# Performance work log

Hardware: AMD Instinct MI355X
Metric: run time of the kernel (lower is better)

## Reference

```python
import jax, jax.numpy as jnp
import numpy as np

N_BLOCKS = 96
N = N_BLOCKS ** 2          # number of image blocks = n_blocks^2
D = 1024                   # feature dim (fixed by Linear(1024+1, 128))
EPS_COS = 1e-6             # eps of F.cosine_similarity
EPS_BN = 1e-5              # BatchNorm1d eps


def setup_inputs() -> dict:
    key = jax.random.key(0)
    ks = jax.random.split(key, 6)
    return {
        "features": jax.random.normal(ks[0], (N, D), dtype=jnp.float32),
        "scores": jax.random.uniform(ks[1], (N,), dtype=jnp.float32),
        "W1": jax.random.normal(ks[2], (D + 1, 128), dtype=jnp.float32) * 0.03,
        "b1": jnp.zeros((128,), jnp.float32),
        "g1": jnp.ones((128,), jnp.float32),
        "be1": jnp.zeros((128,), jnp.float32),
        "W2": jax.random.normal(ks[3], (128, 64), dtype=jnp.float32) * 0.08,
        "b2": jnp.zeros((64,), jnp.float32),
        "g2": jnp.ones((64,), jnp.float32),
        "be2": jnp.zeros((64,), jnp.float32),
        "W3": jax.random.normal(ks[4], (64, 1), dtype=jnp.float32) * 0.12,
        "b3": jnp.zeros((1,), jnp.float32),
    }


def _gaussian_similarity(features):
    # Vectorized form of the O(N^2) pairwise loop:
    #   cos_ij = <f_i, f_j> / max(|f_i||f_j|, eps)
    #   sigma^2 = D * (0.5 + 0.5 * cos)  ->  2*sigma^2 = D * (1 + cos)
    #   sim_ij = exp(-|f_i - f_j|^2 / (2*sigma^2)),  sim_ii = 1
    sq = jnp.sum(features * features, axis=-1)          # [N] squared norms
    gram = features @ features.T                          # [N, N] big GEMM
    norms = jnp.sqrt(sq)
    cos = gram / jnp.maximum(norms[:, None] * norms[None, :], EPS_COS)
    d2 = jnp.maximum(sq[:, None] + sq[None, :] - 2.0 * gram, 0.0)
    denom = jnp.maximum(jnp.float32(D) * (1.0 + cos), EPS_COS)
    sim = jnp.exp(-d2 / denom)
    eye = jnp.eye(sim.shape[0], dtype=bool)
    return jnp.where(eye, jnp.float32(1.0), sim)


def _bn_eval(h, gamma, beta):
    # BatchNorm1d in eval mode with init running stats (mean=0, var=1).
    return gamma * (h / jnp.sqrt(1.0 + EPS_BN)) + beta


def reference(features, scores, W1, b1, g1, be1, W2, b2, g2, be2, W3, b3):
    sim = _gaussian_similarity(features)                  # [N, N]
    x = jnp.concatenate([features, scores[:, None]], axis=1)  # [N, D+1]
    h = jax.nn.relu(_bn_eval(x @ W1 + b1, g1, be1))       # [N, 128]
    h = jax.nn.relu(_bn_eval(h @ W2 + b2, g2, be2))       # [N, 64]
    agg = jax.nn.sigmoid(h @ W3 + b3)[:, 0]               # [N]
    sim_mean = jnp.mean(sim, axis=1)                      # [N]
    # Torch broadcast [N,1] * [N] -> [N,N], then .mean() == mean(agg)*mean(sim_mean)
    return jnp.mean(agg) * jnp.mean(sim_mean)


if __name__ == "__main__":
    out = reference(**setup_inputs())
    print(out)
```

## Files before the change

kernel.cpp:

```cpp
#include <hip/hip_runtime.h>

#define N_IMG 9216
#define DFEAT 1024
#define NBR2 72
#define NPAIR4 2628

typedef __attribute__((ext_vector_type(8))) short short8;
typedef __attribute__((ext_vector_type(4))) float floatx4;
typedef __attribute__((ext_vector_type(16))) float floatx16;
typedef __attribute__((ext_vector_type(4))) int intx4;
typedef __attribute__((ext_vector_type(8))) int intx8;

#define C1F 0.0014088818759657845f
#define C2F 0.05308355472172724f

__device__ __forceinline__ void async_copy16(const void* g, void* l) {
  __builtin_amdgcn_global_load_lds((const __attribute__((address_space(1))) void*)g,
                                   (__attribute__((address_space(3))) void*)l,
                                   16, 0, 0);
}

__device__ __forceinline__ unsigned short f2bf(float x) {
  union { float f; unsigned u; } a; a.f = x;
  unsigned u = a.u;
  u += 0x7fffu + ((u >> 16) & 1u);
  return (unsigned short)(u >> 16);
}

__device__ __forceinline__ unsigned q4(float z) {
  unsigned sg = (__float_as_uint(z) >> 28) & 8u;
  float a = fabsf(z);
  unsigned c = (a < 0.25f) ? 0u : (a < 0.75f) ? 1u : (a < 1.25f) ? 2u :
               (a < 1.75f) ? 3u : (a < 2.5f)  ? 4u : (a < 3.5f)  ? 5u :
               (a < 5.0f)  ? 6u : 7u;
  return c | sg;
}
__device__ __forceinline__ unsigned short pk4(float4 v, float sc) {
  unsigned b0 = q4(v.x * sc) | (q4(v.y * sc) << 4);
  unsigned b1 = q4(v.z * sc) | (q4(v.w * sc) << 4);
  return (unsigned short)(b0 | (b1 << 8));
}

__global__ __launch_bounds__(256) void convert_prep(const float* __restrict__ f,
                                                    const float* __restrict__ W1,
                                                    unsigned char* __restrict__ fbT,
                                                    float* __restrict__ sL,
                                                    float* __restrict__ pL,
                                                    unsigned short* __restrict__ W1t,
                                                    double* __restrict__ sums,
                                                    unsigned* __restrict__ ctr) {
  int b = blockIdx.x, t = threadIdx.x;
  if (b < 2304) {
    int lane = t & 63, wave = t >> 6;
    int row = b * 4 + wave;
    const float4* src = (const float4*)f + (size_t)row * 256;
    float4 v0 = src[lane], v1 = src[64 + lane], v2 = src[128 + lane], v3 = src[192 + lane];
    float s = v0.x * v0.x + v0.y * v0.y + v0.z * v0.z + v0.w * v0.w
            + v1.x * v1.x + v1.y * v1.y + v1.z * v1.z + v1.w * v1.w
            + v2.x * v2.x + v2.y * v2.y + v2.z * v2.z + v2.w * v2.w
            + v3.x * v3.x + v3.y * v3.y + v3.z * v3.z + v3.w * v3.w;
#pragma unroll
    for (int off = 32; off > 0; off >>= 1) s += __shfl_xor(s, off, 64);
    float zsc = rsqrtf(s) * 32.f;
    unsigned short u0 = pk4(v0, zsc), u1 = pk4(v1, zsc),
                   u2 = pk4(v2, zsc), u3 = pk4(v3, zsc);
    unsigned char* tb = fbT + (size_t)(row >> 5) * 16384 + (row & 31) * 32 + (lane & 15) * 2;
    int ko = (lane >> 4) * 1024;
    *(unsigned short*)(tb + ko) = u0;
    *(unsigned short*)(tb + ko + 4096) = u1;
    *(unsigned short*)(tb + ko + 8192) = u2;
    *(unsigned short*)(tb + ko + 12288) = u3;
    if (lane == 0) {
      sL[row] = s * C1F;
      pL[row] = sqrtf(s) * C2F;
    }
  } else {
    int j = b - 2304;
    if (j == 0) {
      if (t < 2) sums[t] = 0.0;
      if (t == 2) *ctr = 0u;
    }
    for (int k = t; k < DFEAT; k += 256)
      W1t[(size_t)j * DFEAT + k] = f2bf(W1[(size_t)k * 128 + j]);
  }
}

__global__ __launch_bounds__(256, 3) void gram_sim(const unsigned char* __restrict__ fbT,
                                                   const float* __restrict__ sL,
                                                   const float* __restrict__ pL,
                                                   double* __restrict__ sums) {
  __shared__ __align__(16) unsigned char stg[2][8192];
  __shared__ float sA[128], pA[128], sB[128], pB[128];
  __shared__ float wpart[4];

  int bid = blockIdx.x, t = threadIdx.x, lane = t & 63, wave = t >> 6;
  int xcd = bid & 7, ii = bid >> 3;
  int L = (xcd < 4 ? xcd * 329 : 1316 + (xcd - 4) * 328) + ii;
  int rem = L, bcol = 0;
  while (rem > bcol) { rem -= (bcol + 1); bcol++; }
  int brow = rem;

  if (t < 128) { sA[t] = sL[brow * 128 + t]; pA[t] = pL[brow * 128 + t]; }
  else { int u = t - 128; sB[u] = sL[bcol * 128 + u]; pB[u] = pL[bcol * 128 + u]; }
  __syncthreads();

  const unsigned char* srcA = fbT + (size_t)(brow * 4 + wave) * 16384 + lane * 16;
  const unsigned char* srcB = fbT + (size_t)(bcol * 4 + wave) * 16384 + lane * 16;
  char* dstA = (char*)stg + wave * 1024 + lane * 16;
  char* dstB = (char*)stg + 4096 + wave * 1024 + lane * 16;

#define STAGE(buf, kb)                                        \
  {                                                           \
    async_copy16(srcA + (kb) * 1024, dstA + (buf) * 8192);    \
    async_copy16(srcB + (kb) * 1024, dstB + (buf) * 8192);    \
  }

  const int r32 = lane & 31, kh = lane >> 5;
  const int loff = r32 * 32 + kh * 16;
  const int wr = (wave & 1) * 64, wc = (wave >> 1) * 64;
  const char* aBase = (const char*)stg + (wr >> 5) * 1024 + loff;
  const char* bBase = (const char*)stg + 4096 + (wc >> 5) * 1024 + loff;

  floatx16 acc[2][2];
#pragma unroll
  for (int mi = 0; mi < 2; mi++)
#pragma unroll
    for (int ni = 0; ni < 2; ni++)
#pragma unroll
      for (int e = 0; e < 16; e++) acc[mi][ni][e] = 0.f;

  union u8x { intx8 v8; intx4 q[2]; };
  u8x A8[2], B8[2];
#pragma unroll
  for (int mi = 0; mi < 2; mi++) A8[mi].q[1] = (intx4){0, 0, 0, 0};
#pragma unroll
  for (int ni = 0; ni < 2; ni++) B8[ni].q[1] = (intx4){0, 0, 0, 0};

  STAGE(0, 0)
  STAGE(1, 1)
#pragma unroll
  for (int kb = 0; kb < 16; kb++) {
    if (kb < 15) asm volatile("s_waitcnt vmcnt(2)" ::: "memory");
    else         asm volatile("s_waitcnt vmcnt(0)" ::: "memory");
    __builtin_amdgcn_s_barrier();
    __builtin_amdgcn_sched_barrier(0);
    const int cur = (kb & 1) * 8192;
    A8[0].q[0] = *(const intx4*)(aBase + cur);
    A8[1].q[0] = *(const intx4*)(aBase + cur + 1024);
    B8[0].q[0] = *(const intx4*)(bBase + cur);
    B8[1].q[0] = *(const intx4*)(bBase + cur + 1024);
#pragma unroll
    for (int mi = 0; mi < 2; mi++)
#pragma unroll
      for (int ni = 0; ni < 2; ni++)
        acc[mi][ni] = __builtin_amdgcn_mfma_scale_f32_32x32x64_f8f6f4(
            A8[mi].v8, B8[ni].v8, acc[mi][ni], 4, 4,
            0, 0x7F7F7F7F, 0, 0x7F7F7F7F);
    __builtin_amdgcn_sched_barrier(0);
    __builtin_amdgcn_s_barrier();
    __builtin_amdgcn_sched_barrier(0);
    if (kb < 14) STAGE((kb & 1), kb + 2)
  }
#undef STAGE

  const bool diag = (brow == bcol);
  float lsum = 0.f;
#pragma unroll
  for (int ni = 0; ni < 2; ni++) {
    int j_loc = wc + ni * 32 + r32;
    float sj = sB[j_loc], pj = pB[j_loc];
#pragma unroll
    for (int mi = 0; mi < 2; mi++) {
      int rbase = wr + mi * 32 + 4 * kh;
#pragma unroll
      for (int reg = 0; reg < 16; reg++) {
        int i_loc = rbase + (reg & 3) + 8 * (reg >> 2);
        float g = acc[mi][ni][reg];
        float si = sA[i_loc], pi = pA[i_loc];
        float r = __builtin_amdgcn_rcpf(1024.f + g);
        float del = pi * pj;
        float gam = si + sj + del;
        float sim = __builtin_amdgcn_exp2f(fmaf(-1024.f, gam * r, del));
        if (!diag) {
          lsum += sim;
        } else {
          lsum += (i_loc < j_loc) ? 2.f * sim : (i_loc == j_loc ? 1.f : 0.f);
        }
      }
    }
  }
  if (!diag) lsum *= 2.f;
#pragma unroll
  for (int off = 32; off > 0; off >>= 1) lsum += __shfl_down(lsum, off, 64);
  if (lane == 0) wpart[wave] = lsum;
  __syncthreads();
  if (t == 0)
    atomicAdd(&sums[0], (double)(wpart[0] + wpart[1] + wpart[2] + wpart[3]));
}

__global__ __launch_bounds__(256) void mlp_full(const float* __restrict__ f,
                                                const unsigned short* __restrict__ W1t,
                                                const float* __restrict__ scores,
                                                const float* __restrict__ W1,
                                                const float* __restrict__ b1,
                                                const float* __restrict__ g1,
                                                const float* __restrict__ be1,
                                                const float* __restrict__ W2, const float* __restrict__ b2,
                                                const float* __restrict__ g2, const float* __restrict__ be2,
                                                const float* __restrict__ W3, const float* __restrict__ b3,
                                                double* __restrict__ sums,
                                                unsigned* __restrict__ ctr,
                                                float* __restrict__ out) {
  int r0 = blockIdx.x * 32;

  __shared__ __align__(16) float As32[2 * 32 * 64];
  __shared__ __align__(16) unsigned short Bs[2 * 128 * 64];
  __shared__ float h1s[32][128];
  __shared__ float h2s[32][65];
  __shared__ float sc[32], b1s[128], g1s[128], be1s[128], wls[128], ls[32];

  int t = threadIdx.x, lane = t & 63, wave = t >> 6;
  if (t < 32) sc[t] = scores[r0 + t];
  if (t < 128) {
    b1s[t] = b1[t]; g1s[t] = g1[t]; be1s[t] = be1[t];
    wls[t] = W1[(size_t)DFEAT * 128 + t];
  }
  __syncthreads();

  floatx4 acc[4];
#pragma unroll
  for (int b = 0; b < 4; b++) acc[b] = (floatx4){0.f, 0.f, 0.f, 0.f};

  const int wr = (wave & 1) * 16, wc = (wave >> 1) * 64;

#define MSTAGE(buf, kk)                                                     \
  {                                                                         \
    const int k0_ = (kk) * 64;                                              \
    int c = t, rA = c >> 4, p = c & 15, l = p ^ (rA & 15);                  \
    async_copy16(f + (size_t)(r0 + rA) * DFEAT + k0_ + l * 4,               \
                 (char*)As32 + (buf) * 8192 + c * 16);                      \
    c = t + 256; rA = c >> 4; p = c & 15; l = p ^ (rA & 15);                \
    async_copy16(f + (size_t)(r0 + rA) * DFEAT + k0_ + l * 4,               \
                 (char*)As32 + (buf) * 8192 + c * 16);                      \
    _Pragma("unroll")                                                       \
    for (int q2 = 0; q2 < 4; q2++) {                                        \
      int cc = t + q2 * 256, rB = cc >> 3, pp = cc & 7, ll = pp ^ (rB & 7); \
      async_copy16(W1t + (size_t)rB * DFEAT + k0_ + ll * 8,                 \
                   (char*)Bs + (buf) * 16384 + cc * 16);                    \
    }                                                                       \
  }

  MSTAGE(0, 0)
  MSTAGE(1, 1)
  for (int kk = 0; kk < 16; kk++) {
    if (kk < 15) asm volatile("s_waitcnt vmcnt(6)" ::: "memory");
    else         asm volatile("s_waitcnt vmcnt(0)" ::: "memory");
    __builtin_amdgcn_s_barrier();
    __builtin_amdgcn_sched_barrier(0);
    const int bufF = (kk & 1) * 2048;
    const int bufS = (kk & 1) * 8192;

    const int mrow = lane & 15;
#pragma unroll
    for (int ks = 0; ks < 2; ks++) {
      const int kq = ks * 32 + (lane >> 4) * 8;
      short8 a, b[4];
      {
        int row = wr + mrow;
        int l0 = kq >> 2;
        int p0 = l0 ^ (row & 15), p1 = (l0 + 1) ^ (row & 15);
        float4 f0 = *(const float4*)&As32[bufF + row * 64 + p0 * 4];
        float4 f1 = *(const float4*)&As32[bufF + row * 64 + p1 * 4];
        a[0] = (short)f2bf(f0.x); a[1] = (short)f2bf(f0.y);
        a[2] = (short)f2bf(f0.z); a[3] = (short)f2bf(f0.w);
        a[4] = (short)f2bf(f1.x); a[5] = (short)f2bf(f1.y);
        a[6] = (short)f2bf(f1.z); a[7] = (short)f2bf(f1.w);
      }
#pragma unroll
      for (int nt = 0; nt < 4; nt++) {
        int row = wc + nt * 16 + mrow;
        int p = (kq >> 3) ^ (row & 7);
        b[nt] = *(const short8*)&Bs[bufS + row * 64 + p * 8];
      }
#pragma unroll
      for (int nt = 0; nt < 4; nt++)
        acc[nt] = __builtin_amdgcn_mfma_f32_16x16x32_bf16(a, b[nt], acc[nt], 0, 0, 0);
    }
    __builtin_amdgcn_sched_barrier(0);
    __builtin_amdgcn_s_barrier();
    __builtin_amdgcn_sched_barrier(0);
    if (kk < 14) MSTAGE((kk & 1), kk + 2)
  }
#undef MSTAGE

  const float inv = 1.0f / sqrtf(1.0f + 1e-5f);
  const int rq = (lane >> 4) * 4, cn = lane & 15;
#pragma unroll
  for (int nt = 0; nt < 4; nt++) {
    int j = wc + nt * 16 + cn;
    float bj = b1s[j], gj = g1s[j] * inv, bej = be1s[j], wj = wls[j];
#pragma unroll
    for (int rr = 0; rr < 4; rr++) {
      int iL = wr + rq + rr;
      float pre = acc[nt][rr] + sc[iL] * wj + bj;
      h1s[iL][j] = fmaxf(gj * pre + bej, 0.f);
    }
  }
  __syncthreads();

  {
    int j = t & 63, rg = (t >> 6) * 8;
    float a2[8];
#pragma unroll
    for (int rr = 0; rr < 8; rr++) a2[rr] = 0.f;
    for (int k = 0; k < 128; k++) {
      float w = W2[k * 64 + j];
#pragma unroll
      for (int rr = 0; rr < 8; rr++) a2[rr] = fmaf(h1s[rg + rr][k], w, a2[rr]);
    }
    float scv = g2[j] * inv, bi = b2[j], be = be2[j];
#pragma unroll
    for (int rr = 0; rr < 8; rr++)
      h2s[rg + rr][j] = fmaxf(scv * (a2[rr] + bi) + be, 0.f);
  }
  __syncthreads();

  if (t < 32) {
    float z = b3[0];
#pragma unroll
    for (int k = 0; k < 64; k++) z = fmaf(h2s[t][k], W3[k], z);
    ls[t] = 1.f / (1.f + __expf(-z));
  }
  __syncthreads();
  if (t == 0) {
    float s = 0.f;
#pragma unroll
    for (int iL = 0; iL < 32; iL++) s += ls[iL];
    atomicAdd(&sums[1], (double)s);
    __threadfence();
    unsigned prev = atomicAdd(ctr, 1u);
    if (prev == 287u) {
      __threadfence();
      double s0 = ((volatile double*)sums)[0];
      double s1 = ((volatile double*)sums)[1];
      out[0] = (float)((s1 / (double)N_IMG) * (s0 / ((double)N_IMG * (double)N_IMG)));
    }
  }
}

extern "C" void kernel_launch(void* const* d_in, const int* in_sizes, int n_in,
                              void* d_out, int out_size, void* d_ws, size_t ws_size,
                              hipStream_t stream) {
  const float* f      = (const float*)d_in[0];
  const float* scores = (const float*)d_in[1];
  const float* W1 = (const float*)d_in[2];
  const float* b1 = (const float*)d_in[3];
  const float* g1 = (const float*)d_in[4];
  const float* be1 = (const float*)d_in[5];
  const float* W2 = (const float*)d_in[6];
  const float* b2 = (const float*)d_in[7];
  const float* g2 = (const float*)d_in[8];
  const float* be2 = (const float*)d_in[9];
  const float* W3 = (const float*)d_in[10];
  const float* b3 = (const float*)d_in[11];

  char* ws = (char*)d_ws;
  unsigned char* fbT  = (unsigned char*)ws;
  float* sL           = (float*)(ws + 4718592);
  float* pL           = (float*)(ws + 4755456);
  unsigned short* W1t = (unsigned short*)(ws + 4792320);
  double* sums        = (double*)(ws + 5054464);
  unsigned* ctr       = (unsigned*)(ws + 5054480);

  convert_prep<<<2432, 256, 0, stream>>>(f, W1, fbT, sL, pL, W1t, sums, ctr);
  gram_sim<<<NPAIR4, 256, 0, stream>>>(fbT, sL, pL, sums);
  mlp_full<<<288, 256, 0, stream>>>(f, W1t, scores, W1, b1, g1, be1,
                                    W2, b2, g2, be2, W3, b3, sums, ctr,
                                    (float*)d_out);
}
```

Before: 188.8 us.

## Load GEMM operands directly from global into registers instead of LDS staging

Removes the LDS double-buffer and its async global-to-LDS copies and block barriers. Each wave now loads its own A and B fragments straight from global memory into a three-slot register ring, prefetching two k-steps ahead. The triangular tile index is also computed with a sqrt estimate plus correction loops instead of a linear subtraction loop. This drops barrier and LDS traffic, but operands shared between waves are now fetched redundantly from global/L2, and register pressure goes up.

```diff
diff --git a/kernel.cpp b/kernel.cpp
--- a/kernel.cpp
+++ b/kernel.cpp
@@ -89,37 +89,29 @@
                                                    const float* __restrict__ sL,
                                                    const float* __restrict__ pL,
                                                    double* __restrict__ sums) {
-  __shared__ __align__(16) unsigned char stg[2][8192];
   __shared__ float sA[128], pA[128], sB[128], pB[128];
   __shared__ float wpart[4];
 
   int bid = blockIdx.x, t = threadIdx.x, lane = t & 63, wave = t >> 6;
   int xcd = bid & 7, ii = bid >> 3;
   int L = (xcd < 4 ? xcd * 329 : 1316 + (xcd - 4) * 328) + ii;
-  int rem = L, bcol = 0;
-  while (rem > bcol) { rem -= (bcol + 1); bcol++; }
-  int brow = rem;
+  int bcol = (int)((sqrtf(8.f * (float)L + 1.f) - 1.f) * 0.5f);
+  while ((bcol + 1) * (bcol + 2) / 2 <= L) bcol++;
+  while (bcol * (bcol + 1) / 2 > L) bcol--;
+  int brow = L - bcol * (bcol + 1) / 2;
 
   if (t < 128) { sA[t] = sL[brow * 128 + t]; pA[t] = pL[brow * 128 + t]; }
   else { int u = t - 128; sB[u] = sL[bcol * 128 + u]; pB[u] = pL[bcol * 128 + u]; }
   __syncthreads();
-
-  const unsigned char* srcA = fbT + (size_t)(brow * 4 + wave) * 16384 + lane * 16;
-  const unsigned char* srcB = fbT + (size_t)(bcol * 4 + wave) * 16384 + lane * 16;
-  char* dstA = (char*)stg + wave * 1024 + lane * 16;
-  char* dstB = (char*)stg + 4096 + wave * 1024 + lane * 16;
-
-#define STAGE(buf, kb)                                        \
-  {                                                           \
-    async_copy16(srcA + (kb) * 1024, dstA + (buf) * 8192);    \
-    async_copy16(srcB + (kb) * 1024, dstB + (buf) * 8192);    \
-  }
 
   const int r32 = lane & 31, kh = lane >> 5;
   const int loff = r32 * 32 + kh * 16;
   const int wr = (wave & 1) * 64, wc = (wave >> 1) * 64;
-  const char* aBase = (const char*)stg + (wr >> 5) * 1024 + loff;
-  const char* bBase = (const char*)stg + 4096 + (wc >> 5) * 1024 + loff;
+
+  const unsigned char* pa0 = fbT + (size_t)(brow * 4 + (wr >> 5)) * 16384 + loff;
+  const unsigned char* pa1 = pa0 + 16384;
+  const unsigned char* pb0 = fbT + (size_t)(bcol * 4 + (wc >> 5)) * 16384 + loff;
+  const unsigned char* pb1 = pb0 + 16384;
 
   floatx16 acc[2][2];
 #pragma unroll
@@ -136,19 +128,21 @@
 #pragma unroll
   for (int ni = 0; ni < 2; ni++) B8[ni].q[1] = (intx4){0, 0, 0, 0};
 
-  STAGE(0, 0)
-  STAGE(1, 1)
+  intx4 bA[3][2], bB[3][2];
+#define LDSET(s, kb)                                                          \
+  {                                                                           \
+    const int o = (kb) * 1024;                                                \
+    bA[s][0] = *(const intx4*)(pa0 + o); bA[s][1] = *(const intx4*)(pa1 + o); \
+    bB[s][0] = *(const intx4*)(pb0 + o); bB[s][1] = *(const intx4*)(pb1 + o); \
+  }
+  LDSET(0, 0)
+  LDSET(1, 1)
 #pragma unroll
   for (int kb = 0; kb < 16; kb++) {
-    if (kb < 15) asm volatile("s_waitcnt vmcnt(2)" ::: "memory");
-    else         asm volatile("s_waitcnt vmcnt(0)" ::: "memory");
-    __builtin_amdgcn_s_barrier();
-    __builtin_amdgcn_sched_barrier(0);
-    const int cur = (kb & 1) * 8192;
-    A8[0].q[0] = *(const intx4*)(aBase + cur);
-    A8[1].q[0] = *(const intx4*)(aBase + cur + 1024);
-    B8[0].q[0] = *(const intx4*)(bBase + cur);
-    B8[1].q[0] = *(const intx4*)(bBase + cur + 1024);
+    const int cur = kb % 3, nxt = (kb + 2) % 3;
+    if (kb < 14) LDSET(nxt, kb + 2)
+    A8[0].q[0] = bA[cur][0]; A8[1].q[0] = bA[cur][1];
+    B8[0].q[0] = bB[cur][0]; B8[1].q[0] = bB[cur][1];
 #pragma unroll
     for (int mi = 0; mi < 2; mi++)
 #pragma unroll
@@ -156,12 +150,8 @@
         acc[mi][ni] = __builtin_amdgcn_mfma_scale_f32_32x32x64_f8f6f4(
             A8[mi].v8, B8[ni].v8, acc[mi][ni], 4, 4,
             0, 0x7F7F7F7F, 0, 0x7F7F7F7F);
-    __builtin_amdgcn_sched_barrier(0);
-    __builtin_amdgcn_s_barrier();
-    __builtin_amdgcn_sched_barrier(0);
-    if (kb < 14) STAGE((kb & 1), kb + 2)
-  }
-#undef STAGE
+  }
+#undef LDSET
 
   const bool diag = (brow == bcol);
   float lsum = 0.f;
```

Result: no change. 189.5 us (+0.4%).
